# Kernel optimization log

Hardware: AMD Instinct MI355X
Metric: run time of the kernel (lower is better)

The kernel has to match this reference:

```python
import jax, jax.numpy as jnp
import numpy as np
from jax import lax

# dims: B=batch, T=seq_len, D=inputSize, H=hiddenSize, L=num_layers, N=3 cell nodes
B, T, D, H, L = 128, 64, 256, 256, 2
WSCALE = 0.05  # scale on randn weight init for numerical health (math unchanged)


def setup_inputs() -> dict:
    key = jax.random.key(0)
    ks = jax.random.split(key, 8)
    return {
        "x": jax.random.normal(ks[0], (B, T, D), dtype=jnp.float32),
        "hidden": jax.random.normal(ks[1], (L, B, H), dtype=jnp.float32),
        # per-timestep cell parameters (the torch module instantiates one cell per timestep)
        "Win0": jax.random.normal(ks[2], (T, D, H), dtype=jnp.float32) * WSCALE,
        "Wh0": jax.random.normal(ks[3], (T, 3, H, H), dtype=jnp.float32) * WSCALE,
        "b0": jax.random.normal(ks[4], (T, 3, H), dtype=jnp.float32) * WSCALE,
        "Win1": jax.random.normal(ks[5], (T, H, H), dtype=jnp.float32) * WSCALE,
        "Wh1": jax.random.normal(ks[6], (T, 3, H, H), dtype=jnp.float32) * WSCALE,
        "b1": jax.random.normal(ks[7], (T, 3, H), dtype=jnp.float32) * WSCALE,
    }


def _cell(xt, h, Win, Wh, b):
    # cellList=[0,0,1,0,2]: activations [tanh, relu, sigmoid], connections [0, 0]
    n0 = jnp.tanh(xt @ Win + h @ Wh[0] + b[0])          # node 0
    n1 = jax.nn.relu(n0 @ Wh[1] + b[1]) + n0            # node 1 (+ node 0 via connection)
    n2 = jax.nn.sigmoid(n1 @ Wh[2] + b[2]) + n0         # node 2 (+ node 0 via connection)
    # unconnected nodes = {1, 2} -> mean over their values
    return 0.5 * (n1 + n2)


def _run_layer(xs_tbd, h0, Win, Wh, b):
    def step(h, inp):
        xt, Wi, Whh, bt = inp
        hn = _cell(xt, h, Wi, Whh, bt)
        return hn, hn
    h_last, outs = lax.scan(step, h0, (xs_tbd, Win, Wh, b))
    return outs, h_last  # outs: [T,B,H]


def reference(x, hidden, Win0, Wh0, b0, Win1, Wh1, b1):
    x_t = jnp.transpose(x, (1, 0, 2))                    # [T,B,D] (batch_first input)
    out0, h0f = _run_layer(x_t, hidden[0], Win0, Wh0, b0)
    out1, h1f = _run_layer(out0, hidden[1], Win1, Wh1, b1)
    output = jnp.transpose(out1, (1, 0, 2))              # [B,T,H], batch_first
    hidden_out = jnp.stack([h0f, h1f], axis=0)           # [L,B,H]
    return output, hidden_out
```

## Files before the change

kernel.cpp:

```cpp
#include <hip/hip_runtime.h>


typedef _Float16 f16;
typedef __attribute__((ext_vector_type(8))) _Float16 f16x8;
typedef __attribute__((ext_vector_type(4))) float f32x4;
typedef __attribute__((ext_vector_type(4))) float float4v;

#define Tt 64
#define FLAG_MAGIC 0x52570000

#define WS_WH0T   0
#define WS_WIN1T  25165824
#define WS_WH1T   33554432
#define WS_WIN0T  58720256
#define WS_XW     67108864
#define WS_P3     75497472
#define WS_FLAGS  83886080

__device__ __forceinline__ void sb() { __builtin_amdgcn_sched_barrier(0); }

template <int N>
__device__ __forceinline__ void waitvm() {
  __builtin_amdgcn_s_waitcnt(0x0F70 | (N & 15) | ((N >> 4) << 14));
}
__device__ __forceinline__ void waitlgkm0() { __builtin_amdgcn_s_waitcnt(0xC07F); }

__device__ __forceinline__ void barx() {
  asm volatile("s_waitcnt lgkmcnt(0)\n\ts_barrier" ::: "memory");
}

__device__ __forceinline__ void dma16(const void* g, void* l) {
  __builtin_amdgcn_global_load_lds(
      (const __attribute__((address_space(1))) unsigned int*)g,
      (__attribute__((address_space(3))) unsigned int*)l, 16, 0, 0);
}

__device__ __forceinline__ float tanh_fast(float x) {
  float xc = fminf(fmaxf(x, -15.f), 15.f);
  float e = __expf(2.f * xc);
  return (e - 1.f) / (e + 1.f);
}
__device__ __forceinline__ float sigmoid_fast(float x) { return 1.f / (1.f + __expf(-x)); }

__global__ __launch_bounds__(256) void transpose_cvt_kernel(
    const float* __restrict__ Wh0, const float* __restrict__ Win1,
    const float* __restrict__ Wh1, const float* __restrict__ Win0,
    f16* __restrict__ Wh0T, f16* __restrict__ Win1T, f16* __restrict__ Wh1T,
    f16* __restrict__ Win0T) {
  __shared__ float tile[256 * 33];
  const int bid = blockIdx.x;
  const int mat = bid >> 3, n0 = (bid & 7) << 5;
  const float* src; f16* dst;
  if (mat < 192)      { src = Wh0  + (size_t)mat * 65536;         dst = Wh0T  + (size_t)mat * 65536; }
  else if (mat < 256) { src = Win1 + (size_t)(mat - 192) * 65536; dst = Win1T + (size_t)(mat - 192) * 65536; }
  else if (mat < 448) { src = Wh1  + (size_t)(mat - 256) * 65536; dst = Wh1T  + (size_t)(mat - 256) * 65536; }
  else                { src = Win0 + (size_t)(mat - 448) * 65536; dst = Win0T + (size_t)(mat - 448) * 65536; }
  const int tid = threadIdx.x;
  const int c2 = tid & 15, kl = tid >> 4;
#pragma unroll
  for (int p = 0; p < 16; ++p) {
    const int k = kl + p * 16;
    float2 v = *(const float2*)(src + k * 256 + n0 + c2 * 2);
    tile[k * 33 + c2 * 2]     = v.x;
    tile[k * 33 + c2 * 2 + 1] = v.y;
  }
  __syncthreads();
  const int n = tid >> 5, c = tid & 31;
#pragma unroll
  for (int it = 0; it < 4; ++it) {
    const int nn = n + it * 8;
    f16x8 vv;
#pragma unroll
    for (int i = 0; i < 8; ++i) vv[i] = (f16)tile[(c * 8 + i) * 33 + nn];
    *(f16x8*)((char*)dst + (size_t)(n0 + nn) * 512 + c * 16) = vv;
  }
}

__global__ __launch_bounds__(512, 2) void xw_kernel(
    const float* __restrict__ x, const f16* __restrict__ Win0T,
    const float* __restrict__ b0, float* __restrict__ xw) {
  const int t = blockIdx.x >> 3, bb = blockIdx.x & 7;
  const int rb = bb << 4;
  const int tid = threadIdx.x, lane = tid & 63, w = tid >> 6;
  const int q = lane >> 4, mn = lane & 15, dr = q * 4;
  const f16* wt = Win0T + (size_t)t * 65536;
  const float4v* xr = (const float4v*)(x + ((size_t)(rb + mn) * Tt + t) * 256);
  f32x4 acc[2] = {{0.f,0.f,0.f,0.f},{0.f,0.f,0.f,0.f}};
#pragma unroll
  for (int kt = 0; kt < 8; ++kt) {
    const int k0 = kt * 32 + q * 8;
    float4v x0 = xr[k0 / 4], x1 = xr[k0 / 4 + 1];
    f16x8 a = {(f16)x0.x, (f16)x0.y, (f16)x0.z, (f16)x0.w,
               (f16)x1.x, (f16)x1.y, (f16)x1.z, (f16)x1.w};
#pragma unroll
    for (int nt = 0; nt < 2; ++nt) {
      f16x8 b = *(const f16x8*)(wt + (size_t)(w * 32 + nt * 16 + mn) * 256 + k0);
      acc[nt] = __builtin_amdgcn_mfma_f32_16x16x32_f16(a, b, acc[nt], 0, 0, 0);
    }
  }
#pragma unroll
  for (int nt = 0; nt < 2; ++nt) {
    const int n = w * 32 + nt * 16 + mn;
    const float bv = b0[(size_t)t * 768 + n];
#pragma unroll
    for (int r = 0; r < 4; ++r)
      xw[(size_t)t * 32768 + (size_t)(rb + dr + r) * 256 + n] = acc[nt][r] + bv;
  }
}

template <int NW, bool DMA>
__device__ __forceinline__ void phase(f32x4 (&acc)[2], const char* arow, const char* wb,
                                      const int (&bo)[4], const char* gnext, char* lnext,
                                      const int (&off)[8], int q) {
  waitvm<NW>();
  sb();
  f16x8 a[4], b[8];
#pragma unroll
  for (int kt = 0; kt < 4; ++kt) {
    a[kt]         = *(const f16x8*)(arow + kt * 64 + q * 16);
    b[kt * 2]     = *(const f16x8*)(wb + bo[kt]);
    b[kt * 2 + 1] = *(const f16x8*)(wb + bo[kt] + 4096);
  }
  sb();
  waitlgkm0();
  if (DMA) {
#pragma unroll
    for (int d = 0; d < 8; ++d) dma16(gnext + off[d], lnext + d * 1024);
  }
  sb();
#pragma unroll
  for (int kt = 0; kt < 4; ++kt) {
    acc[0] = __builtin_amdgcn_mfma_f32_16x16x32_f16(a[kt], b[kt * 2],     acc[0], 0, 0, 0);
    acc[1] = __builtin_amdgcn_mfma_f32_16x16x32_f16(a[kt], b[kt * 2 + 1], acc[1], 0, 0, 0);
  }
}

__global__ __launch_bounds__(512, 1) void rnn_kernel(
    const float* __restrict__ hidden,
    const f16* __restrict__ Wh0T, const float* __restrict__ b0,
    const f16* __restrict__ Win1T, const f16* __restrict__ Wh1T, const float* __restrict__ b1,
    const float* __restrict__ xw, float* __restrict__ p3seq, int* __restrict__ flags,
    float* __restrict__ out) {
  __shared__ __align__(16) char smem[147968];
  char* wlds = smem;
  char* abuf = smem + 131072;
  char* nbuf = smem + 139520;

  const int tid = threadIdx.x;
  const int lane = tid & 63;
  const int w = tid >> 6;
  const int q = lane >> 4;
  const int mn = lane & 15;
  const bool isL0 = blockIdx.x < 8;
  const int g = blockIdx.x & 7;
  const int rb = g << 4;
  const int nc = w * 32 + mn;
  const int dr = q * 4;
  const int wslice = w * 16384;

  int off[8], bo[4];
#pragma unroll
  for (int d = 0; d < 8; ++d) {
    const int row = 4 * d + q;
    off[d] = row * 512 + ((mn ^ (row & 15)) << 4);
  }
#pragma unroll
  for (int kt = 0; kt < 4; ++kt)
    bo[kt] = mn * 256 + (((kt * 4 + q) ^ mn) << 4);

  const float* hsrc = hidden + (isL0 ? 0 : 32768) + (size_t)rb * 256;
  for (int i = tid; i < 16 * 256; i += 512) {
    const int m = i >> 8, n = i & 255;
    *(f16*)(abuf + m * 528 + n * 2) = (f16)hsrc[m * 256 + n];
  }

  char* bufA = wlds + wslice;
  char* bufB = bufA + 8192;
  const f32x4 zero4 = {0.f, 0.f, 0.f, 0.f};
  float n0v[2][4], n1v[2][4];

  if (isL0) {
    const char* WB = (const char*)Wh0T;
    const char* WI = (const char*)Win1T;
    {
      const char* gw = WB + wslice;
#pragma unroll
      for (int d = 0; d < 8; ++d) dma16(gw + off[d], bufA + d * 1024);
#pragma unroll
      for (int d = 0; d < 8; ++d) dma16(gw + 256 + off[d], bufB + d * 1024);
      sb();
    }
    barx();

#pragma unroll 1
    for (int t = 0; t < Tt; ++t) {
      const int tn = (t < Tt - 1) ? t + 1 : t;
      const bool last = (t == Tt - 1);
      const char* wt  = WB + (size_t)t * 393216 + wslice;
      const char* wtn = WB + (size_t)tn * 393216 + wslice;
      const char* wit = WI + (size_t)t * 131072 + wslice;

      float xwv[2][4];
#pragma unroll
      for (int nt = 0; nt < 2; ++nt)
#pragma unroll
        for (int r = 0; r < 4; ++r)
          xwv[nt][r] = xw[(size_t)t * 32768 + (size_t)(rb + dr + r) * 256 + nc + nt * 16];
      const float bv1a = b0[(size_t)t * 768 + 256 + nc], bv1b = b0[(size_t)t * 768 + 256 + nc + 16];
      const float bv2a = b0[(size_t)t * 768 + 512 + nc], bv2b = b0[(size_t)t * 768 + 512 + nc + 16];
      const float p3ba = b1[(size_t)t * 768 + nc],       p3bb = b1[(size_t)t * 768 + nc + 16];
      sb();

      f32x4 acc[2];
      acc[0] = zero4; acc[1] = zero4;
      phase<22, true>(acc, abuf + mn * 528,       bufA, bo, wt + 131072,       bufA, off, q);
      phase<22, true>(acc, abuf + mn * 528 + 256, bufB, bo, wt + 131072 + 256, bufB, off, q);
      waitvm<16>();
      sb();
#pragma unroll
      for (int nt = 0; nt < 2; ++nt)
#pragma unroll
        for (int r = 0; r < 4; ++r) {
          float v = tanh_fast(acc[nt][r] + xwv[nt][r]);
          n0v[nt][r] = v;
          *(f16*)(nbuf + (dr + r) * 528 + (nc + nt * 16) * 2) = (f16)v;
        }
      barx();

      acc[0] = zero4; acc[1] = zero4;
      phase<8, true>(acc, nbuf + mn * 528,       bufA, bo, wt + 262144,       bufA, off, q);
      phase<8, true>(acc, nbuf + mn * 528 + 256, bufB, bo, wt + 262144 + 256, bufB, off, q);
      barx();
#pragma unroll
      for (int nt = 0; nt < 2; ++nt) {
        const float bv = nt ? bv1b : bv1a;
#pragma unroll
        for (int r = 0; r < 4; ++r) {
          float v = fmaxf(acc[nt][r] + bv, 0.f) + n0v[nt][r];
          n1v[nt][r] = v;
          *(f16*)(nbuf + (dr + r) * 528 + (nc + nt * 16) * 2) = (f16)v;
        }
      }
      barx();

      acc[0] = zero4; acc[1] = zero4;
      phase<8, true>(acc, nbuf + mn * 528,       bufA, bo, wit,       bufA, off, q);
      phase<8, true>(acc, nbuf + mn * 528 + 256, bufB, bo, wit + 256, bufB, off, q);
#pragma unroll
      for (int nt = 0; nt < 2; ++nt) {
        const float bv = nt ? bv2b : bv2a;
#pragma unroll
        for (int r = 0; r < 4; ++r) {
          float s = sigmoid_fast(acc[nt][r] + bv);
          float hv = 0.5f * (n1v[nt][r] + s + n0v[nt][r]);
          *(f16*)(abuf + (dr + r) * 528 + (nc + nt * 16) * 2) = (f16)hv;
          if (last) out[2097152 + (size_t)(rb + dr + r) * 256 + nc + nt * 16] = hv;
        }
      }
      barx();

      acc[0] = zero4; acc[1] = zero4;
      phase<8, false>(acc, abuf + mn * 528,       bufA, bo, wt, bufA, off, q);
      phase<0, false>(acc, abuf + mn * 528 + 256, bufB, bo, wt, bufB, off, q);
#pragma unroll
      for (int nt = 0; nt < 2; ++nt) {
        const float bv = nt ? p3bb : p3ba;
#pragma unroll
        for (int r = 0; r < 4; ++r)
          p3seq[(size_t)(g * 64 + t) * 4096 + (dr + r) * 256 + nc + nt * 16] =
              acc[nt][r] + bv;
      }
      waitvm<0>();
      __threadfence();
      __syncthreads();
      if (tid == 0) {
        __hip_atomic_store(&flags[g * 64 + t], FLAG_MAGIC | (t + 1),
                           __ATOMIC_RELEASE, __HIP_MEMORY_SCOPE_AGENT);
      }
      sb();
      {
        const char* gw = wtn;
#pragma unroll
        for (int d = 0; d < 8; ++d) dma16(gw + off[d], bufA + d * 1024);
#pragma unroll
        for (int d = 0; d < 8; ++d) dma16(gw + 256 + off[d], bufB + d * 1024);
        sb();
      }
    }
  } else {
    const char* WH = (const char*)Wh1T;
    const float* p3g = p3seq + (size_t)g * 64 * 4096;
    {
      const char* gw = WH + wslice;
#pragma unroll
      for (int d = 0; d < 8; ++d) dma16(gw + off[d], bufA + d * 1024);
#pragma unroll
      for (int d = 0; d < 8; ++d) dma16(gw + 256 + off[d], bufB + d * 1024);
      sb();
      waitvm<0>();
    }
    barx();

#pragma unroll 1
    for (int t = 0; t < Tt; ++t) {
      const int tn = (t < Tt - 1) ? t + 1 : t;
      const bool last = (t == Tt - 1);
      const char* wht = WH + (size_t)t * 393216 + wslice;
      const char* whn = WH + (size_t)tn * 393216 + wslice;

      f32x4 acc[2];
      acc[0] = zero4; acc[1] = zero4;
      phase<17, true>(acc, abuf + mn * 528,       bufA, bo, wht + 131072,       bufA, off, q);
      phase<9,  true>(acc, abuf + mn * 528 + 256, bufB, bo, wht + 131072 + 256, bufB, off, q);

      {
        const int want = FLAG_MAGIC | (t + 1);
        while (__hip_atomic_load(&flags[g * 64 + t], __ATOMIC_ACQUIRE,
                                 __HIP_MEMORY_SCOPE_AGENT) != want) {}
      }
      sb();
      float p3v[2][4];
#pragma unroll
      for (int nt = 0; nt < 2; ++nt)
#pragma unroll
        for (int r = 0; r < 4; ++r)
          p3v[nt][r] = p3g[(size_t)t * 4096 + (dr + r) * 256 + nc + nt * 16];
      const float bv1a = b1[(size_t)t * 768 + 256 + nc], bv1b = b1[(size_t)t * 768 + 256 + nc + 16];
      const float bv2a = b1[(size_t)t * 768 + 512 + nc], bv2b = b1[(size_t)t * 768 + 512 + nc + 16];
      sb();
      waitvm<0>();
      sb();
#pragma unroll
      for (int nt = 0; nt < 2; ++nt)
#pragma unroll
        for (int r = 0; r < 4; ++r) {
          float v = tanh_fast(acc[nt][r] + p3v[nt][r]);
          n0v[nt][r] = v;
          *(f16*)(nbuf + (dr + r) * 528 + (nc + nt * 16) * 2) = (f16)v;
        }
      barx();

      acc[0] = zero4; acc[1] = zero4;
      phase<63, true>(acc, nbuf + mn * 528,       bufA, bo, wht + 262144,       bufA, off, q);
      phase<63, true>(acc, nbuf + mn * 528 + 256, bufB, bo, wht + 262144 + 256, bufB, off, q);
      barx();
#pragma unroll
      for (int nt = 0; nt < 2; ++nt) {
        const float bv = nt ? bv1b : bv1a;
#pragma unroll
        for (int r = 0; r < 4; ++r) {
          float v = fmaxf(acc[nt][r] + bv, 0.f) + n0v[nt][r];
          n1v[nt][r] = v;
          *(f16*)(nbuf + (dr + r) * 528 + (nc + nt * 16) * 2) = (f16)v;
        }
      }
      barx();

      acc[0] = zero4; acc[1] = zero4;
      phase<8, true>(acc, nbuf + mn * 528,       bufA, bo, whn,       bufA, off, q);
      phase<8, true>(acc, nbuf + mn * 528 + 256, bufB, bo, whn + 256, bufB, off, q);
#pragma unroll
      for (int nt = 0; nt < 2; ++nt) {
        const float bv = nt ? bv2b : bv2a;
#pragma unroll
        for (int r = 0; r < 4; ++r) {
          float s = sigmoid_fast(acc[nt][r] + bv);
          float hv = 0.5f * (n1v[nt][r] + s + n0v[nt][r]);
          *(f16*)(abuf + (dr + r) * 528 + (nc + nt * 16) * 2) = (f16)hv;
          out[((size_t)(rb + dr + r) * Tt + t) * 256 + nc + nt * 16] = hv;
          if (last) out[2097152 + 32768 + (size_t)(rb + dr + r) * 256 + nc + nt * 16] = hv;
        }
      }
      barx();
    }
  }
}

extern "C" void kernel_launch(void* const* d_in, const int* in_sizes, int n_in,
                              void* d_out, int out_size, void* d_ws, size_t ws_size,
                              hipStream_t stream) {
  (void)in_sizes; (void)n_in; (void)out_size; (void)ws_size;
  const float* x      = (const float*)d_in[0];
  const float* hidden = (const float*)d_in[1];
  const float* Win0   = (const float*)d_in[2];
  const float* Wh0    = (const float*)d_in[3];
  const float* b0     = (const float*)d_in[4];
  const float* Win1   = (const float*)d_in[5];
  const float* Wh1    = (const float*)d_in[6];
  const float* b1     = (const float*)d_in[7];
  float* out = (float*)d_out;

  char* ws = (char*)d_ws;
  f16* Wh0T   = (f16*)(ws + WS_WH0T);
  f16* Win1T  = (f16*)(ws + WS_WIN1T);
  f16* Wh1T   = (f16*)(ws + WS_WH1T);
  f16* Win0T  = (f16*)(ws + WS_WIN0T);
  float* xwp  = (float*)(ws + WS_XW);
  float* p3p  = (float*)(ws + WS_P3);
  int* flags  = (int*)(ws + WS_FLAGS);

  transpose_cvt_kernel<<<dim3(4096), dim3(256), 0, stream>>>(
      Wh0, Win1, Wh1, Win0, Wh0T, Win1T, Wh1T, Win0T);
  xw_kernel<<<dim3(512), dim3(512), 0, stream>>>(x, Win0T, b0, xwp);
  rnn_kernel<<<dim3(16), dim3(512), 0, stream>>>(
      hidden, Wh0T, b0, Win1T, Wh1T, b1, xwp, p3p, flags, out);
}
```

Before: 804.5 us.

## Split layer-1 input projection between producer and consumer blocks with ping-pong weight buffers

Layer-0 blocks now compute only the first K-half of the layer-1 input projection (Win1 @ h). They also publish the f16 hidden state for the upper half of the columns to a new workspace buffer. Layer-1 blocks compute the remaining K-half themselves from that f16 hidden copy and stream the extra Win1 slice ahead of the flag wait. Weight LDS staging buffers swap roles each step so prefetches overlap across phases, and the per-step threadfence is dropped. This aims to shorten the producer's critical path and balance the two layers. It risks memory-ordering issues and relies on fragile hand-tuned vmcnt waits.

```diff
diff --git a/kernel.cpp b/kernel.cpp
--- a/kernel.cpp
+++ b/kernel.cpp
@@ -14,8 +14,9 @@
 #define WS_WH1T   33554432
 #define WS_WIN0T  58720256
 #define WS_XW     67108864
-#define WS_P3     75497472
-#define WS_FLAGS  83886080
+#define WS_P3A    75497472
+#define WS_HSEQH  83886080
+#define WS_FLAGS  85983232
 
 __device__ __forceinline__ void sb() { __builtin_amdgcn_sched_barrier(0); }
 
@@ -139,8 +140,8 @@
     const float* __restrict__ hidden,
     const f16* __restrict__ Wh0T, const float* __restrict__ b0,
     const f16* __restrict__ Win1T, const f16* __restrict__ Wh1T, const float* __restrict__ b1,
-    const float* __restrict__ xw, float* __restrict__ p3seq, int* __restrict__ flags,
-    float* __restrict__ out) {
+    const float* __restrict__ xw, float* __restrict__ p3a, f16* __restrict__ hseqh,
+    int* __restrict__ flags, float* __restrict__ out) {
   __shared__ __align__(16) char smem[147968];
   char* wlds = smem;
   char* abuf = smem + 131072;
@@ -174,8 +175,8 @@
     *(f16*)(abuf + m * 528 + n * 2) = (f16)hsrc[m * 256 + n];
   }
 
-  char* bufA = wlds + wslice;
-  char* bufB = bufA + 8192;
+  char* pA = wlds + wslice;
+  char* pB = pA + 8192;
   const f32x4 zero4 = {0.f, 0.f, 0.f, 0.f};
   float n0v[2][4], n1v[2][4];
 
@@ -185,10 +186,11 @@
     {
       const char* gw = WB + wslice;
 #pragma unroll
-      for (int d = 0; d < 8; ++d) dma16(gw + off[d], bufA + d * 1024);
-#pragma unroll
-      for (int d = 0; d < 8; ++d) dma16(gw + 256 + off[d], bufB + d * 1024);
-      sb();
+      for (int d = 0; d < 8; ++d) dma16(gw + off[d], pA + d * 1024);
+#pragma unroll
+      for (int d = 0; d < 8; ++d) dma16(gw + 256 + off[d], pB + d * 1024);
+      sb();
+      waitvm<0>();
     }
     barx();
 
@@ -213,8 +215,8 @@
 
       f32x4 acc[2];
       acc[0] = zero4; acc[1] = zero4;
-      phase<22, true>(acc, abuf + mn * 528,       bufA, bo, wt + 131072,       bufA, off, q);
-      phase<22, true>(acc, abuf + mn * 528 + 256, bufB, bo, wt + 131072 + 256, bufB, off, q);
+      phase<22, true>(acc, abuf + mn * 528,       pA, bo, wt + 131072,       pA, off, q);
+      phase<22, true>(acc, abuf + mn * 528 + 256, pB, bo, wt + 131072 + 256, pB, off, q);
       waitvm<16>();
       sb();
 #pragma unroll
@@ -228,8 +230,8 @@
       barx();
 
       acc[0] = zero4; acc[1] = zero4;
-      phase<8, true>(acc, nbuf + mn * 528,       bufA, bo, wt + 262144,       bufA, off, q);
-      phase<8, true>(acc, nbuf + mn * 528 + 256, bufB, bo, wt + 262144 + 256, bufB, off, q);
+      phase<8, true>(acc, nbuf + mn * 528,       pA, bo, wt + 262144,       pA, off, q);
+      phase<8, true>(acc, nbuf + mn * 528 + 256, pB, bo, wt + 262144 + 256, pB, off, q);
       barx();
 #pragma unroll
       for (int nt = 0; nt < 2; ++nt) {
@@ -244,8 +246,8 @@
       barx();
 
       acc[0] = zero4; acc[1] = zero4;
-      phase<8, true>(acc, nbuf + mn * 528,       bufA, bo, wit,       bufA, off, q);
-      phase<8, true>(acc, nbuf + mn * 528 + 256, bufB, bo, wit + 256, bufB, off, q);
+      phase<8, true>(acc, nbuf + mn * 528,       pA, bo, wit, pA, off, q);
+      phase<8, true>(acc, nbuf + mn * 528 + 256, pB, bo, wtn, pB, off, q);
 #pragma unroll
       for (int nt = 0; nt < 2; ++nt) {
         const float bv = nt ? bv2b : bv2a;
@@ -259,19 +261,44 @@
       }
       barx();
 
-      acc[0] = zero4; acc[1] = zero4;
-      phase<8, false>(acc, abuf + mn * 528,       bufA, bo, wt, bufA, off, q);
-      phase<0, false>(acc, abuf + mn * 528 + 256, bufB, bo, wt, bufB, off, q);
+      waitvm<8>();
+      sb();
+      {
+        f16x8 a3[4], b3[8];
+#pragma unroll
+        for (int kt = 0; kt < 4; ++kt) {
+          a3[kt]         = *(const f16x8*)(abuf + mn * 528 + kt * 64 + q * 16);
+          b3[kt * 2]     = *(const f16x8*)(pA + bo[kt]);
+          b3[kt * 2 + 1] = *(const f16x8*)(pA + bo[kt] + 4096);
+        }
+        sb();
+        waitlgkm0();
+        sb();
+        acc[0] = zero4; acc[1] = zero4;
+#pragma unroll
+        for (int kt = 0; kt < 4; ++kt) {
+          acc[0] = __builtin_amdgcn_mfma_f32_16x16x32_f16(a3[kt], b3[kt * 2],     acc[0], 0, 0, 0);
+          acc[1] = __builtin_amdgcn_mfma_f32_16x16x32_f16(a3[kt], b3[kt * 2 + 1], acc[1], 0, 0, 0);
+        }
+      }
 #pragma unroll
       for (int nt = 0; nt < 2; ++nt) {
         const float bv = nt ? p3bb : p3ba;
 #pragma unroll
         for (int r = 0; r < 4; ++r)
-          p3seq[(size_t)(g * 64 + t) * 4096 + (dr + r) * 256 + nc + nt * 16] =
-              acc[nt][r] + bv;
-      }
+          p3a[(size_t)(g * 64 + t) * 4096 + (dr + r) * 256 + nc + nt * 16] = acc[nt][r] + bv;
+      }
+      if (w >= 4) {
+        char* hs = (char*)hseqh + (size_t)(g * 64 + t) * 4096;
+#pragma unroll
+        for (int nt = 0; nt < 2; ++nt)
+#pragma unroll
+          for (int r = 0; r < 4; ++r)
+            *(f16*)(hs + (dr + r) * 256 + (nc + nt * 16 - 128) * 2) =
+                *(f16*)(abuf + (dr + r) * 528 + (nc + nt * 16) * 2);
+      }
+      sb();
       waitvm<0>();
-      __threadfence();
       __syncthreads();
       if (tid == 0) {
         __hip_atomic_store(&flags[g * 64 + t], FLAG_MAGIC | (t + 1),
@@ -279,23 +306,23 @@
       }
       sb();
       {
-        const char* gw = wtn;
-#pragma unroll
-        for (int d = 0; d < 8; ++d) dma16(gw + off[d], bufA + d * 1024);
-#pragma unroll
-        for (int d = 0; d < 8; ++d) dma16(gw + 256 + off[d], bufB + d * 1024);
+#pragma unroll
+        for (int d = 0; d < 8; ++d) dma16(wtn + 256 + off[d], pA + d * 1024);
         sb();
       }
+      { char* tp = pA; pA = pB; pB = tp; }
     }
   } else {
     const char* WH = (const char*)Wh1T;
-    const float* p3g = p3seq + (size_t)g * 64 * 4096;
+    const char* WI = (const char*)Win1T;
+    const float* p3g = p3a + (size_t)g * 64 * 4096;
+    const char* hsg = (const char*)hseqh + (size_t)g * 64 * 4096;
     {
       const char* gw = WH + wslice;
 #pragma unroll
-      for (int d = 0; d < 8; ++d) dma16(gw + off[d], bufA + d * 1024);
-#pragma unroll
-      for (int d = 0; d < 8; ++d) dma16(gw + 256 + off[d], bufB + d * 1024);
+      for (int d = 0; d < 8; ++d) dma16(gw + off[d], pA + d * 1024);
+#pragma unroll
+      for (int d = 0; d < 8; ++d) dma16(gw + 256 + off[d], pB + d * 1024);
       sb();
       waitvm<0>();
     }
@@ -307,11 +334,16 @@
       const bool last = (t == Tt - 1);
       const char* wht = WH + (size_t)t * 393216 + wslice;
       const char* whn = WH + (size_t)tn * 393216 + wslice;
+      const char* wit = WI + (size_t)t * 131072 + wslice;
+
+      const float bv1a = b1[(size_t)t * 768 + 256 + nc], bv1b = b1[(size_t)t * 768 + 256 + nc + 16];
+      const float bv2a = b1[(size_t)t * 768 + 512 + nc], bv2b = b1[(size_t)t * 768 + 512 + nc + 16];
+      sb();
 
       f32x4 acc[2];
       acc[0] = zero4; acc[1] = zero4;
-      phase<17, true>(acc, abuf + mn * 528,       bufA, bo, wht + 131072,       bufA, off, q);
-      phase<9,  true>(acc, abuf + mn * 528 + 256, bufB, bo, wht + 131072 + 256, bufB, off, q);
+      phase<12, true>(acc, abuf + mn * 528,       pA, bo, wit + 256,    pA, off, q);
+      phase<12, true>(acc, abuf + mn * 528 + 256, pB, bo, wht + 131072, pB, off, q);
 
       {
         const int want = FLAG_MAGIC | (t + 1);
@@ -319,17 +351,37 @@
                                  __HIP_MEMORY_SCOPE_AGENT) != want) {}
       }
       sb();
+      const char* ht = hsg + (size_t)t * 4096;
+      f16x8 af[4];
+#pragma unroll
+      for (int kt = 0; kt < 4; ++kt)
+        af[kt] = *(const f16x8*)(ht + mn * 256 + kt * 64 + q * 16);
       float p3v[2][4];
 #pragma unroll
       for (int nt = 0; nt < 2; ++nt)
 #pragma unroll
         for (int r = 0; r < 4; ++r)
           p3v[nt][r] = p3g[(size_t)t * 4096 + (dr + r) * 256 + nc + nt * 16];
-      const float bv1a = b1[(size_t)t * 768 + 256 + nc], bv1b = b1[(size_t)t * 768 + 256 + nc + 16];
-      const float bv2a = b1[(size_t)t * 768 + 512 + nc], bv2b = b1[(size_t)t * 768 + 512 + nc + 16];
-      sb();
-      waitvm<0>();
-      sb();
+      sb();
+
+      {
+        f16x8 b3[8];
+#pragma unroll
+        for (int kt = 0; kt < 4; ++kt) {
+          b3[kt * 2]     = *(const f16x8*)(pA + bo[kt]);
+          b3[kt * 2 + 1] = *(const f16x8*)(pA + bo[kt] + 4096);
+        }
+        sb();
+        waitlgkm0();
+#pragma unroll
+        for (int d = 0; d < 8; ++d) dma16(wht + 131072 + 256 + off[d], pA + d * 1024);
+        sb();
+#pragma unroll
+        for (int kt = 0; kt < 4; ++kt) {
+          acc[0] = __builtin_amdgcn_mfma_f32_16x16x32_f16(af[kt], b3[kt * 2],     acc[0], 0, 0, 0);
+          acc[1] = __builtin_amdgcn_mfma_f32_16x16x32_f16(af[kt], b3[kt * 2 + 1], acc[1], 0, 0, 0);
+        }
+      }
 #pragma unroll
       for (int nt = 0; nt < 2; ++nt)
 #pragma unroll
@@ -341,8 +393,8 @@
       barx();
 
       acc[0] = zero4; acc[1] = zero4;
-      phase<63, true>(acc, nbuf + mn * 528,       bufA, bo, wht + 262144,       bufA, off, q);
-      phase<63, true>(acc, nbuf + mn * 528 + 256, bufB, bo, wht + 262144 + 256, bufB, off, q);
+      phase<63, true>(acc, nbuf + mn * 528,       pB, bo, wht + 262144,       pB, off, q);
+      phase<8,  true>(acc, nbuf + mn * 528 + 256, pA, bo, wht + 262144 + 256, pA, off, q);
       barx();
 #pragma unroll
       for (int nt = 0; nt < 2; ++nt) {
@@ -357,8 +409,8 @@
       barx();
 
       acc[0] = zero4; acc[1] = zero4;
-      phase<8, true>(acc, nbuf + mn * 528,       bufA, bo, whn,       bufA, off, q);
-      phase<8, true>(acc, nbuf + mn * 528 + 256, bufB, bo, whn + 256, bufB, off, q);
+      phase<8, true>(acc, nbuf + mn * 528,       pB, bo, whn,       pB, off, q);
+      phase<8, true>(acc, nbuf + mn * 528 + 256, pA, bo, whn + 256, pA, off, q);
 #pragma unroll
       for (int nt = 0; nt < 2; ++nt) {
         const float bv = nt ? bv2b : bv2a;
@@ -372,6 +424,7 @@
         }
       }
       barx();
+      { char* tp = pA; pA = pB; pB = tp; }
     }
   }
 }
@@ -396,12 +449,13 @@
   f16* Wh1T   = (f16*)(ws + WS_WH1T);
   f16* Win0T  = (f16*)(ws + WS_WIN0T);
   float* xwp  = (float*)(ws + WS_XW);
-  float* p3p  = (float*)(ws + WS_P3);
+  float* p3p  = (float*)(ws + WS_P3A);
+  f16* hseqh  = (f16*)(ws + WS_HSEQH);
   int* flags  = (int*)(ws + WS_FLAGS);
 
   transpose_cvt_kernel<<<dim3(4096), dim3(256), 0, stream>>>(
       Wh0, Win1, Wh1, Win0, Wh0T, Win1T, Wh1T, Win0T);
   xw_kernel<<<dim3(512), dim3(512), 0, stream>>>(x, Win0T, b0, xwp);
   rnn_kernel<<<dim3(16), dim3(512), 0, stream>>>(
-      hidden, Wh0T, b0, Win1T, Wh1T, b1, xwp, p3p, flags, out);
-}
+      hidden, Wh0T, b0, Win1T, Wh1T, b1, xwp, p3p, hseqh, flags, out);
+}
```

Result: faster. 685.0 us (-14.9%).

## Pipeline recurrence as per-timestep weight-stationary blocks linked by flags

Applied to the files above, without the earlier changes.

Replaces the 16-block recurrence kernel, which streamed each timestep's weights through LDS, with 192 blocks. Each block owns one timestep and one stage (layer-0 cell, layer-1 input projection, layer-1 cell) and keeps that timestep's weights resident in LDS and registers. The 8 batch groups flow through these blocks as a wavefront pipeline, handing off hidden states through global f16 sequence buffers and release/acquire flags. The aim is to stop re-streaming weights on the serial critical path and to spread the work over many more CUs. In exchange it adds cross-block global round-trips and spin-waits on every handoff, and it assumes all 192 blocks are co-resident. The spin loop is also capped, so a block that waits too long proceeds silently.

```diff
diff --git a/kernel.cpp b/kernel.cpp
--- a/kernel.cpp
+++ b/kernel.cpp
@@ -14,8 +14,10 @@
 #define WS_WH1T   33554432
 #define WS_WIN0T  58720256
 #define WS_XW     67108864
-#define WS_P3     75497472
-#define WS_FLAGS  83886080
+#define WS_H0SEQ  75497472
+#define WS_P3SEQ  79691776
+#define WS_H1SEQ  88080384
+#define WS_FLAGS  92274688
 
 __device__ __forceinline__ void sb() { __builtin_amdgcn_sched_barrier(0); }
 
@@ -41,6 +43,12 @@
   return (e - 1.f) / (e + 1.f);
 }
 __device__ __forceinline__ float sigmoid_fast(float x) { return 1.f / (1.f + __expf(-x)); }
+
+__device__ __forceinline__ void acquire(const int* f, int want) {
+  for (int i = 0; i < (1 << 20); ++i) {
+    if (__hip_atomic_load(f, __ATOMIC_ACQUIRE, __HIP_MEMORY_SCOPE_AGENT) == want) return;
+  }
+}
 
 __global__ __launch_bounds__(256) void transpose_cvt_kernel(
     const float* __restrict__ Wh0, const float* __restrict__ Win1,
@@ -108,55 +116,57 @@
   }
 }
 
-template <int NW, bool DMA>
-__device__ __forceinline__ void phase(f32x4 (&acc)[2], const char* arow, const char* wb,
-                                      const int (&bo)[4], const char* gnext, char* lnext,
-                                      const int (&off)[8], int q) {
-  waitvm<NW>();
-  sb();
-  f16x8 a[4], b[8];
+__device__ __forceinline__ void mmLDS(f32x4 (&acc)[2], const f16x8* af,
+                                      const char* lw, const int (&bo)[4]) {
+  f16x8 b[8];
 #pragma unroll
   for (int kt = 0; kt < 4; ++kt) {
-    a[kt]         = *(const f16x8*)(arow + kt * 64 + q * 16);
-    b[kt * 2]     = *(const f16x8*)(wb + bo[kt]);
-    b[kt * 2 + 1] = *(const f16x8*)(wb + bo[kt] + 4096);
+    b[kt * 2]     = *(const f16x8*)(lw + bo[kt]);
+    b[kt * 2 + 1] = *(const f16x8*)(lw + bo[kt] + 4096);
   }
   sb();
   waitlgkm0();
-  if (DMA) {
-#pragma unroll
-    for (int d = 0; d < 8; ++d) dma16(gnext + off[d], lnext + d * 1024);
-  }
   sb();
 #pragma unroll
   for (int kt = 0; kt < 4; ++kt) {
-    acc[0] = __builtin_amdgcn_mfma_f32_16x16x32_f16(a[kt], b[kt * 2],     acc[0], 0, 0, 0);
-    acc[1] = __builtin_amdgcn_mfma_f32_16x16x32_f16(a[kt], b[kt * 2 + 1], acc[1], 0, 0, 0);
-  }
-}
-
-__global__ __launch_bounds__(512, 1) void rnn_kernel(
+    acc[0] = __builtin_amdgcn_mfma_f32_16x16x32_f16(af[kt], b[kt * 2],     acc[0], 0, 0, 0);
+    acc[1] = __builtin_amdgcn_mfma_f32_16x16x32_f16(af[kt], b[kt * 2 + 1], acc[1], 0, 0, 0);
+  }
+}
+
+__device__ __forceinline__ void mmREG(f32x4 (&acc)[2], const char* nrow,
+                                      const f16x8 (&wr)[16], int q) {
+  f16x8 a[8];
+#pragma unroll
+  for (int kt = 0; kt < 8; ++kt)
+    a[kt] = *(const f16x8*)(nrow + kt * 64 + q * 16);
+  sb();
+  waitlgkm0();
+  sb();
+#pragma unroll
+  for (int kt = 0; kt < 8; ++kt) {
+    acc[0] = __builtin_amdgcn_mfma_f32_16x16x32_f16(a[kt], wr[kt],     acc[0], 0, 0, 0);
+    acc[1] = __builtin_amdgcn_mfma_f32_16x16x32_f16(a[kt], wr[8 + kt], acc[1], 0, 0, 0);
+  }
+}
+
+__global__ __launch_bounds__(512, 2) void stage_kernel(
     const float* __restrict__ hidden,
     const f16* __restrict__ Wh0T, const float* __restrict__ b0,
-    const f16* __restrict__ Win1T, const f16* __restrict__ Wh1T, const float* __restrict__ b1,
-    const float* __restrict__ xw, float* __restrict__ p3seq, int* __restrict__ flags,
-    float* __restrict__ out) {
-  __shared__ __align__(16) char smem[147968];
-  char* wlds = smem;
-  char* abuf = smem + 131072;
-  char* nbuf = smem + 139520;
-
-  const int tid = threadIdx.x;
-  const int lane = tid & 63;
-  const int w = tid >> 6;
-  const int q = lane >> 4;
-  const int mn = lane & 15;
-  const bool isL0 = blockIdx.x < 8;
-  const int g = blockIdx.x & 7;
-  const int rb = g << 4;
-  const int nc = w * 32 + mn;
-  const int dr = q * 4;
-  const int wslice = w * 16384;
+    const f16* __restrict__ Win1T, const f16* __restrict__ Wh1T,
+    const float* __restrict__ b1, const float* __restrict__ xw,
+    f16* __restrict__ h0seq, float* __restrict__ p3seq, f16* __restrict__ h1seq,
+    int* __restrict__ flags, float* __restrict__ out) {
+  __shared__ __align__(16) char smem[139520];
+  char* ldsW = smem;
+  char* nbuf = smem + 131072;
+
+  const int tid = threadIdx.x, lane = tid & 63, w = tid >> 6;
+  const int q = lane >> 4, mn = lane & 15;
+  const int dr = q * 4, nc = w * 32 + mn;
+  const int wsl = w * 16384;
+  char* lwA = ldsW + wsl;
+  char* lwB = lwA + 8192;
 
   int off[8], bo[4];
 #pragma unroll
@@ -168,55 +178,80 @@
   for (int kt = 0; kt < 4; ++kt)
     bo[kt] = mn * 256 + (((kt * 4 + q) ^ mn) << 4);
 
-  const float* hsrc = hidden + (isL0 ? 0 : 32768) + (size_t)rb * 256;
-  for (int i = tid; i < 16 * 256; i += 512) {
-    const int m = i >> 8, n = i & 255;
-    *(f16*)(abuf + m * 528 + n * 2) = (f16)hsrc[m * 256 + n];
-  }
-
-  char* bufA = wlds + wslice;
-  char* bufB = bufA + 8192;
+  const int bid = blockIdx.x;
+  const int kind = bid >> 6;
+  const int t = bid & 63;
+  const bool lastT = (t == Tt - 1);
+  const int tag = FLAG_MAGIC | (t + 1);
+
+  int* fL0 = flags;
+  int* fM3 = flags + 512;
+  int* fL1 = flags + 1024;
+
   const f32x4 zero4 = {0.f, 0.f, 0.f, 0.f};
-  float n0v[2][4], n1v[2][4];
-
-  if (isL0) {
-    const char* WB = (const char*)Wh0T;
-    const char* WI = (const char*)Win1T;
+
+  if (kind == 0) {
+    const char* WB = (const char*)Wh0T + (size_t)t * 393216;
     {
-      const char* gw = WB + wslice;
-#pragma unroll
-      for (int d = 0; d < 8; ++d) dma16(gw + off[d], bufA + d * 1024);
-#pragma unroll
-      for (int d = 0; d < 8; ++d) dma16(gw + 256 + off[d], bufB + d * 1024);
-      sb();
-    }
+#pragma unroll
+      for (int d = 0; d < 8; ++d) dma16(WB + wsl + off[d], lwA + d * 1024);
+#pragma unroll
+      for (int d = 0; d < 8; ++d) dma16(WB + wsl + 256 + off[d], lwB + d * 1024);
+    }
+    f16x8 w1r[16], w2r[16];
+    {
+      const char* B1 = WB + 131072;
+      const char* B2 = WB + 262144;
+#pragma unroll
+      for (int nt = 0; nt < 2; ++nt)
+#pragma unroll
+        for (int kt = 0; kt < 8; ++kt) {
+          const size_t o = (size_t)(nc + nt * 16) * 512 + kt * 64 + q * 16;
+          w1r[nt * 8 + kt] = *(const f16x8*)(B1 + o);
+          w2r[nt * 8 + kt] = *(const f16x8*)(B2 + o);
+        }
+    }
+    const float bv1a = b0[(size_t)t * 768 + 256 + nc], bv1b = b0[(size_t)t * 768 + 256 + nc + 16];
+    const float bv2a = b0[(size_t)t * 768 + 512 + nc], bv2b = b0[(size_t)t * 768 + 512 + nc + 16];
+    waitvm<0>();
     barx();
 
 #pragma unroll 1
-    for (int t = 0; t < Tt; ++t) {
-      const int tn = (t < Tt - 1) ? t + 1 : t;
-      const bool last = (t == Tt - 1);
-      const char* wt  = WB + (size_t)t * 393216 + wslice;
-      const char* wtn = WB + (size_t)tn * 393216 + wslice;
-      const char* wit = WI + (size_t)t * 131072 + wslice;
-
+    for (int g = 0; g < 8; ++g) {
+      const int rb = g << 4;
+      if (t > 0) acquire(&fL0[g * 64 + t - 1], FLAG_MAGIC | t);
+      sb();
+      f16x8 af[8];
+      if (t > 0) {
+        const char* ht = (const char*)h0seq + (size_t)(g * 64 + t - 1) * 8192;
+#pragma unroll
+        for (int kt = 0; kt < 8; ++kt)
+          af[kt] = *(const f16x8*)(ht + mn * 512 + kt * 64 + q * 16);
+      } else {
+        const float* hp = hidden + (size_t)rb * 256;
+#pragma unroll
+        for (int kt = 0; kt < 8; ++kt) {
+          const float4v* p = (const float4v*)(hp + mn * 256 + kt * 32 + q * 8);
+          float4v x0 = p[0], x1 = p[1];
+          f16x8 v;
+          v[0] = (f16)x0.x; v[1] = (f16)x0.y; v[2] = (f16)x0.z; v[3] = (f16)x0.w;
+          v[4] = (f16)x1.x; v[5] = (f16)x1.y; v[6] = (f16)x1.z; v[7] = (f16)x1.w;
+          af[kt] = v;
+        }
+      }
       float xwv[2][4];
 #pragma unroll
       for (int nt = 0; nt < 2; ++nt)
 #pragma unroll
         for (int r = 0; r < 4; ++r)
           xwv[nt][r] = xw[(size_t)t * 32768 + (size_t)(rb + dr + r) * 256 + nc + nt * 16];
-      const float bv1a = b0[(size_t)t * 768 + 256 + nc], bv1b = b0[(size_t)t * 768 + 256 + nc + 16];
-      const float bv2a = b0[(size_t)t * 768 + 512 + nc], bv2b = b0[(size_t)t * 768 + 512 + nc + 16];
-      const float p3ba = b1[(size_t)t * 768 + nc],       p3bb = b1[(size_t)t * 768 + nc + 16];
       sb();
 
       f32x4 acc[2];
       acc[0] = zero4; acc[1] = zero4;
-      phase<22, true>(acc, abuf + mn * 528,       bufA, bo, wt + 131072,       bufA, off, q);
-      phase<22, true>(acc, abuf + mn * 528 + 256, bufB, bo, wt + 131072 + 256, bufB, off, q);
-      waitvm<16>();
-      sb();
+      mmLDS(acc, af,     lwA, bo);
+      mmLDS(acc, af + 4, lwB, bo);
+      float n0v[2][4], n1v[2][4];
 #pragma unroll
       for (int nt = 0; nt < 2; ++nt)
 #pragma unroll
@@ -228,24 +263,25 @@
       barx();
 
       acc[0] = zero4; acc[1] = zero4;
-      phase<8, true>(acc, nbuf + mn * 528,       bufA, bo, wt + 262144,       bufA, off, q);
-      phase<8, true>(acc, nbuf + mn * 528 + 256, bufB, bo, wt + 262144 + 256, bufB, off, q);
-      barx();
+      mmREG(acc, nbuf + mn * 528, w1r, q);
 #pragma unroll
       for (int nt = 0; nt < 2; ++nt) {
         const float bv = nt ? bv1b : bv1a;
 #pragma unroll
-        for (int r = 0; r < 4; ++r) {
-          float v = fmaxf(acc[nt][r] + bv, 0.f) + n0v[nt][r];
-          n1v[nt][r] = v;
-          *(f16*)(nbuf + (dr + r) * 528 + (nc + nt * 16) * 2) = (f16)v;
-        }
-      }
-      barx();
-
-      acc[0] = zero4; acc[1] = zero4;
-      phase<8, true>(acc, nbuf + mn * 528,       bufA, bo, wit,       bufA, off, q);
-      phase<8, true>(acc, nbuf + mn * 528 + 256, bufB, bo, wit + 256, bufB, off, q);
+        for (int r = 0; r < 4; ++r)
+          n1v[nt][r] = fmaxf(acc[nt][r] + bv, 0.f) + n0v[nt][r];
+      }
+      barx();
+#pragma unroll
+      for (int nt = 0; nt < 2; ++nt)
+#pragma unroll
+        for (int r = 0; r < 4; ++r)
+          *(f16*)(nbuf + (dr + r) * 528 + (nc + nt * 16) * 2) = (f16)n1v[nt][r];
+      barx();
+
+      acc[0] = zero4; acc[1] = zero4;
+      mmREG(acc, nbuf + mn * 528, w2r, q);
+      char* hs = (char*)h0seq + (size_t)(g * 64 + t) * 8192;
 #pragma unroll
       for (int nt = 0; nt < 2; ++nt) {
         const float bv = nt ? bv2b : bv2a;
@@ -253,83 +289,123 @@
         for (int r = 0; r < 4; ++r) {
           float s = sigmoid_fast(acc[nt][r] + bv);
           float hv = 0.5f * (n1v[nt][r] + s + n0v[nt][r]);
-          *(f16*)(abuf + (dr + r) * 528 + (nc + nt * 16) * 2) = (f16)hv;
-          if (last) out[2097152 + (size_t)(rb + dr + r) * 256 + nc + nt * 16] = hv;
-        }
-      }
-      barx();
-
-      acc[0] = zero4; acc[1] = zero4;
-      phase<8, false>(acc, abuf + mn * 528,       bufA, bo, wt, bufA, off, q);
-      phase<0, false>(acc, abuf + mn * 528 + 256, bufB, bo, wt, bufB, off, q);
+          *(f16*)(hs + (dr + r) * 512 + (nc + nt * 16) * 2) = (f16)hv;
+          if (lastT) out[2097152 + (size_t)(rb + dr + r) * 256 + nc + nt * 16] = hv;
+        }
+      }
+      sb();
+      waitvm<0>();
+      __syncthreads();
+      if (tid == 0)
+        __hip_atomic_store(&fL0[g * 64 + t], tag, __ATOMIC_RELEASE, __HIP_MEMORY_SCOPE_AGENT);
+      sb();
+    }
+  } else if (kind == 1) {
+    const char* WB = (const char*)Win1T + (size_t)t * 131072;
+    {
+#pragma unroll
+      for (int d = 0; d < 8; ++d) dma16(WB + wsl + off[d], lwA + d * 1024);
+#pragma unroll
+      for (int d = 0; d < 8; ++d) dma16(WB + wsl + 256 + off[d], lwB + d * 1024);
+    }
+    const float p3ba = b1[(size_t)t * 768 + nc], p3bb = b1[(size_t)t * 768 + nc + 16];
+    waitvm<0>();
+    barx();
+
+#pragma unroll 1
+    for (int g = 0; g < 8; ++g) {
+      acquire(&fL0[g * 64 + t], tag);
+      sb();
+      f16x8 af[8];
+      const char* ht = (const char*)h0seq + (size_t)(g * 64 + t) * 8192;
+#pragma unroll
+      for (int kt = 0; kt < 8; ++kt)
+        af[kt] = *(const f16x8*)(ht + mn * 512 + kt * 64 + q * 16);
+      sb();
+      f32x4 acc[2];
+      acc[0] = zero4; acc[1] = zero4;
+      mmLDS(acc, af,     lwA, bo);
+      mmLDS(acc, af + 4, lwB, bo);
+      float* ps = p3seq + (size_t)(g * 64 + t) * 4096;
 #pragma unroll
       for (int nt = 0; nt < 2; ++nt) {
         const float bv = nt ? p3bb : p3ba;
 #pragma unroll
         for (int r = 0; r < 4; ++r)
-          p3seq[(size_t)(g * 64 + t) * 4096 + (dr + r) * 256 + nc + nt * 16] =
-              acc[nt][r] + bv;
-      }
+          ps[(dr + r) * 256 + nc + nt * 16] = acc[nt][r] + bv;
+      }
+      sb();
       waitvm<0>();
-      __threadfence();
       __syncthreads();
-      if (tid == 0) {
-        __hip_atomic_store(&flags[g * 64 + t], FLAG_MAGIC | (t + 1),
-                           __ATOMIC_RELEASE, __HIP_MEMORY_SCOPE_AGENT);
-      }
-      sb();
-      {
-        const char* gw = wtn;
-#pragma unroll
-        for (int d = 0; d < 8; ++d) dma16(gw + off[d], bufA + d * 1024);
-#pragma unroll
-        for (int d = 0; d < 8; ++d) dma16(gw + 256 + off[d], bufB + d * 1024);
-        sb();
-      }
+      if (tid == 0)
+        __hip_atomic_store(&fM3[g * 64 + t], tag, __ATOMIC_RELEASE, __HIP_MEMORY_SCOPE_AGENT);
+      sb();
     }
   } else {
-    const char* WH = (const char*)Wh1T;
-    const float* p3g = p3seq + (size_t)g * 64 * 4096;
+    const char* WB = (const char*)Wh1T + (size_t)t * 393216;
     {
-      const char* gw = WH + wslice;
-#pragma unroll
-      for (int d = 0; d < 8; ++d) dma16(gw + off[d], bufA + d * 1024);
-#pragma unroll
-      for (int d = 0; d < 8; ++d) dma16(gw + 256 + off[d], bufB + d * 1024);
-      sb();
-      waitvm<0>();
-    }
+#pragma unroll
+      for (int d = 0; d < 8; ++d) dma16(WB + wsl + off[d], lwA + d * 1024);
+#pragma unroll
+      for (int d = 0; d < 8; ++d) dma16(WB + wsl + 256 + off[d], lwB + d * 1024);
+    }
+    f16x8 w1r[16], w2r[16];
+    {
+      const char* B1 = WB + 131072;
+      const char* B2 = WB + 262144;
+#pragma unroll
+      for (int nt = 0; nt < 2; ++nt)
+#pragma unroll
+        for (int kt = 0; kt < 8; ++kt) {
+          const size_t o = (size_t)(nc + nt * 16) * 512 + kt * 64 + q * 16;
+          w1r[nt * 8 + kt] = *(const f16x8*)(B1 + o);
+          w2r[nt * 8 + kt] = *(const f16x8*)(B2 + o);
+        }
+    }
+    const float bv1a = b1[(size_t)t * 768 + 256 + nc], bv1b = b1[(size_t)t * 768 + 256 + nc + 16];
+    const float bv2a = b1[(size_t)t * 768 + 512 + nc], bv2b = b1[(size_t)t * 768 + 512 + nc + 16];
+    waitvm<0>();
     barx();
 
 #pragma unroll 1
-    for (int t = 0; t < Tt; ++t) {
-      const int tn = (t < Tt - 1) ? t + 1 : t;
-      const bool last = (t == Tt - 1);
-      const char* wht = WH + (size_t)t * 393216 + wslice;
-      const char* whn = WH + (size_t)tn * 393216 + wslice;
+    for (int g = 0; g < 8; ++g) {
+      const int rb = g << 4;
+      if (t > 0) acquire(&fL1[g * 64 + t - 1], FLAG_MAGIC | t);
+      sb();
+      f16x8 af[8];
+      if (t > 0) {
+        const char* ht = (const char*)h1seq + (size_t)(g * 64 + t - 1) * 8192;
+#pragma unroll
+        for (int kt = 0; kt < 8; ++kt)
+          af[kt] = *(const f16x8*)(ht + mn * 512 + kt * 64 + q * 16);
+      } else {
+        const float* hp = hidden + 32768 + (size_t)rb * 256;
+#pragma unroll
+        for (int kt = 0; kt < 8; ++kt) {
+          const float4v* p = (const float4v*)(hp + mn * 256 + kt * 32 + q * 8);
+          float4v x0 = p[0], x1 = p[1];
+          f16x8 v;
+          v[0] = (f16)x0.x; v[1] = (f16)x0.y; v[2] = (f16)x0.z; v[3] = (f16)x0.w;
+          v[4] = (f16)x1.x; v[5] = (f16)x1.y; v[6] = (f16)x1.z; v[7] = (f16)x1.w;
+          af[kt] = v;
+        }
+      }
+      acquire(&fM3[g * 64 + t], tag);
+      sb();
+      float p3v[2][4];
+      const float* ps = p3seq + (size_t)(g * 64 + t) * 4096;
+#pragma unroll
+      for (int nt = 0; nt < 2; ++nt)
+#pragma unroll
+        for (int r = 0; r < 4; ++r)
+          p3v[nt][r] = ps[(dr + r) * 256 + nc + nt * 16];
+      sb();
 
       f32x4 acc[2];
       acc[0] = zero4; acc[1] = zero4;
-      phase<17, true>(acc, abuf + mn * 528,       bufA, bo, wht + 131072,       bufA, off, q);
-      phase<9,  true>(acc, abuf + mn * 528 + 256, bufB, bo, wht + 131072 + 256, bufB, off, q);
-
-      {
-        const int want = FLAG_MAGIC | (t + 1);
-        while (__hip_atomic_load(&flags[g * 64 + t], __ATOMIC_ACQUIRE,
-                                 __HIP_MEMORY_SCOPE_AGENT) != want) {}
-      }
-      sb();
-      float p3v[2][4];
-#pragma unroll
-      for (int nt = 0; nt < 2; ++nt)
-#pragma unroll
-        for (int r = 0; r < 4; ++r)
-          p3v[nt][r] = p3g[(size_t)t * 4096 + (dr + r) * 256 + nc + nt * 16];
-      const float bv1a = b1[(size_t)t * 768 + 256 + nc], bv1b = b1[(size_t)t * 768 + 256 + nc + 16];
-      const float bv2a = b1[(size_t)t * 768 + 512 + nc], bv2b = b1[(size_t)t * 768 + 512 + nc + 16];
-      sb();
-      waitvm<0>();
-      sb();
+      mmLDS(acc, af,     lwA, bo);
+      mmLDS(acc, af + 4, lwB, bo);
+      float n0v[2][4], n1v[2][4];
 #pragma unroll
       for (int nt = 0; nt < 2; ++nt)
 #pragma unroll
@@ -341,24 +417,25 @@
       barx();
 
       acc[0] = zero4; acc[1] = zero4;
-      phase<63, true>(acc, nbuf + mn * 528,       bufA, bo, wht + 262144,       bufA, off, q);
-      phase<63, true>(acc, nbuf + mn * 528 + 256, bufB, bo, wht + 262144 + 256, bufB, off, q);
-      barx();
+      mmREG(acc, nbuf + mn * 528, w1r, q);
 #pragma unroll
       for (int nt = 0; nt < 2; ++nt) {
         const float bv = nt ? bv1b : bv1a;
 #pragma unroll
-        for (int r = 0; r < 4; ++r) {
-          float v = fmaxf(acc[nt][r] + bv, 0.f) + n0v[nt][r];
-          n1v[nt][r] = v;
-          *(f16*)(nbuf + (dr + r) * 528 + (nc + nt * 16) * 2) = (f16)v;
-        }
-      }
-      barx();
-
-      acc[0] = zero4; acc[1] = zero4;
-      phase<8, true>(acc, nbuf + mn * 528,       bufA, bo, whn,       bufA, off, q);
-      phase<8, true>(acc, nbuf + mn * 528 + 256, bufB, bo, whn + 256, bufB, off, q);
+        for (int r = 0; r < 4; ++r)
+          n1v[nt][r] = fmaxf(acc[nt][r] + bv, 0.f) + n0v[nt][r];
+      }
+      barx();
+#pragma unroll
+      for (int nt = 0; nt < 2; ++nt)
+#pragma unroll
+        for (int r = 0; r < 4; ++r)
+          *(f16*)(nbuf + (dr + r) * 528 + (nc + nt * 16) * 2) = (f16)n1v[nt][r];
+      barx();
+
+      acc[0] = zero4; acc[1] = zero4;
+      mmREG(acc, nbuf + mn * 528, w2r, q);
+      char* hs = (char*)h1seq + (size_t)(g * 64 + t) * 8192;
 #pragma unroll
       for (int nt = 0; nt < 2; ++nt) {
         const float bv = nt ? bv2b : bv2a;
@@ -366,12 +443,17 @@
         for (int r = 0; r < 4; ++r) {
           float s = sigmoid_fast(acc[nt][r] + bv);
           float hv = 0.5f * (n1v[nt][r] + s + n0v[nt][r]);
-          *(f16*)(abuf + (dr + r) * 528 + (nc + nt * 16) * 2) = (f16)hv;
+          *(f16*)(hs + (dr + r) * 512 + (nc + nt * 16) * 2) = (f16)hv;
           out[((size_t)(rb + dr + r) * Tt + t) * 256 + nc + nt * 16] = hv;
-          if (last) out[2097152 + 32768 + (size_t)(rb + dr + r) * 256 + nc + nt * 16] = hv;
-        }
-      }
-      barx();
+          if (lastT) out[2097152 + 32768 + (size_t)(rb + dr + r) * 256 + nc + nt * 16] = hv;
+        }
+      }
+      sb();
+      waitvm<0>();
+      __syncthreads();
+      if (tid == 0)
+        __hip_atomic_store(&fL1[g * 64 + t], tag, __ATOMIC_RELEASE, __HIP_MEMORY_SCOPE_AGENT);
+      sb();
     }
   }
 }
@@ -396,12 +478,14 @@
   f16* Wh1T   = (f16*)(ws + WS_WH1T);
   f16* Win0T  = (f16*)(ws + WS_WIN0T);
   float* xwp  = (float*)(ws + WS_XW);
-  float* p3p  = (float*)(ws + WS_P3);
+  f16* h0seq  = (f16*)(ws + WS_H0SEQ);
+  float* p3p  = (float*)(ws + WS_P3SEQ);
+  f16* h1seq  = (f16*)(ws + WS_H1SEQ);
   int* flags  = (int*)(ws + WS_FLAGS);
 
   transpose_cvt_kernel<<<dim3(4096), dim3(256), 0, stream>>>(
       Wh0, Win1, Wh1, Win0, Wh0T, Win1T, Wh1T, Win0T);
   xw_kernel<<<dim3(512), dim3(512), 0, stream>>>(x, Win0T, b0, xwp);
-  rnn_kernel<<<dim3(16), dim3(512), 0, stream>>>(
-      hidden, Wh0T, b0, Win1T, Wh1T, b1, xwp, p3p, flags, out);
-}
+  stage_kernel<<<dim3(192), dim3(512), 0, stream>>>(
+      hidden, Wh0T, b0, Win1T, Wh1T, b1, xwp, h0seq, p3p, h1seq, flags, out);
+}
```

Result: slower. 1.517 ms (+88.6%).
